# Kernel optimization log

Hardware: AMD Instinct MI355X
Metric: run time of the kernel (lower is better)

## Reference

```python
import jax, jax.numpy as jnp
import numpy as np

B, C, W, H = 4, 256, 128, 128
BLK = 16
D = C // 8


def setup_inputs() -> dict:
    key = jax.random.key(0)
    ks = jax.random.split(key, 7)
    s = 0.05
    return {
        "x": jax.random.normal(ks[0], (B, C, W, H), jnp.float32),
        "Wq": jax.random.normal(ks[1], (D, C), jnp.float32) * s,
        "bq": jax.random.normal(ks[2], (D,), jnp.float32) * s,
        "Wk": jax.random.normal(ks[3], (D, C), jnp.float32) * s,
        "bk": jax.random.normal(ks[4], (D,), jnp.float32) * s,
        "Wv": jax.random.normal(ks[5], (C, C), jnp.float32) * s,
        "bv": jax.random.normal(ks[6], (C,), jnp.float32) * s,
        "gamma": jnp.full((1,), 0.5, jnp.float32),
    }


def reference(x, Wq, bq, Wk, bk, Wv, bv, gamma):
    Bx, Cx, Wx, Hx = x.shape
    blk = BLK
    pw = (blk - Wx % blk) % blk
    ph = (blk - Hx % blk) % blk
    xp = jnp.pad(x, ((0, 0), (0, 0), (0, pw), (0, ph))) if (pw or ph) else x
    Wp, Hp = xp.shape[2], xp.shape[3]
    nW, nH = Wp // blk, Hp // blk
    N = blk * blk
    # partition into non-overlapping blk x blk windows -> (G, C, N)
    xb = xp.reshape(Bx, Cx, nW, blk, nH, blk).transpose(0, 2, 4, 1, 3, 5)
    xb = xb.reshape(-1, Cx, N)
    # padding mask: positions whose channel-abs-sum is zero are masked out
    mask = jnp.abs(xb).sum(axis=1) > 0  # (G, N) bool
    # 1x1 convs == per-pixel linear projections
    q = jnp.einsum('dc,gcn->gnd', Wq, xb) + bq            # (G, N, D)
    k = jnp.einsum('dc,gcn->gdn', Wk, xb) + bk[:, None]   # (G, D, N)
    energy = jnp.einsum('gnd,gdm->gnm', q, k)             # (G, N, N)
    NEG = jnp.float32(-1e9)
    energy = jnp.where(mask[:, None, :], energy, NEG)  # mask keys
    energy = jnp.where(mask[:, :, None], energy, NEG)  # mask queries
    att = jax.nn.softmax(energy, axis=-1)
    v = jnp.einsum('dc,gcn->gdn', Wv, xb) + bv[:, None]   # (G, C, N)
    out = jnp.einsum('gcm,gnm->gcn', v, att)              # (G, C, N)
    out = out.reshape(Bx, nW, nH, Cx, blk, blk).transpose(0, 3, 1, 4, 2, 5)
    out = out.reshape(Bx, Cx, Wp, Hp)[:, :, :Wx, :Hx]
    out = gamma * out + x
    return out, att
```

## Files before the change

kernel.cpp:

```cpp
#include <hip/hip_runtime.h>

typedef unsigned short u16;
typedef __attribute__((ext_vector_type(8))) short short8;
typedef __attribute__((ext_vector_type(4))) short s16x4;
typedef __attribute__((ext_vector_type(4))) float f32x4;

#define CC 256
#define WW 128
#define HH 128
#define DD 32
#define NN 256
#define WH (WW * HH)
#define P8 524288
#define OUTEL 16777216

__device__ __forceinline__ u16 f2bf(float f) {
  unsigned u = __float_as_uint(f);
  return (u16)((u + 0x7FFFu + ((u >> 16) & 1u)) >> 16);
}
__device__ __forceinline__ float bf2f(u16 h) {
  return __uint_as_float(((unsigned)h) << 16);
}

__global__ __launch_bounds__(256) void k_pack(const float* __restrict__ Wq,
                                              const float* __restrict__ Wk,
                                              float* __restrict__ wqk) {
  int idx = blockIdx.x * 256 + threadIdx.x;
  int r = idx >> 8, c = idx & 255;
  float v = (r < 32) ? Wq[r * 256 + c] : Wk[(r - 32) * 256 + c];
  wqk[c * 64 + r] = v;
}

__global__ __launch_bounds__(1024) void k_qk(const float* __restrict__ x,
                                             const float* __restrict__ wqk,
                                             const float* __restrict__ bq,
                                             const float* __restrict__ bk,
                                             u16* __restrict__ qk,
                                             u16* __restrict__ xbf) {
  __shared__ float xs[2][64 * 256];
  int hw = blockIdx.x;
  int g = (hw & 7) * 32 + (hw >> 3);
  int bb = g >> 6, wb = (g >> 3) & 7, hb = g & 7;
  int w0 = wb * 16, h0 = hb * 16;
  int t = threadIdx.x, ln = t & 63;
  int dg = __builtin_amdgcn_readfirstlane(t >> 6);
  int dq4 = dg & 7, is_k = dg >> 3;
  const float* xwin = x + (size_t)bb * CC * WH + (size_t)w0 * HH + h0;
  u16* xbg = xbf + (size_t)g * CC * NN;

  f32x4 st[4];
#pragma unroll
  for (int j = 0; j < 4; ++j) {
    int lin = j * 1024 + t;
    int c = lin >> 6, sub = lin & 63;
    st[j] = *(const f32x4*)(xwin + (size_t)c * WH + (sub >> 2) * HH + (sub & 3) * 4);
  }
#pragma unroll
  for (int j = 0; j < 4; ++j) {
    int lin = j * 1024 + t;
    int c = lin >> 6, sub = lin & 63;
    *(f32x4*)&xs[0][c * 256 + sub * 4] = st[j];
    s16x4 bp;
#pragma unroll
    for (int i = 0; i < 4; ++i) bp[i] = (short)f2bf(st[j][i]);
    *(s16x4*)&xbg[(size_t)c * NN + sub * 4] = bp;
  }

  float acc[4][4];
#pragma unroll
  for (int j = 0; j < 4; ++j)
#pragma unroll
    for (int i = 0; i < 4; ++i) acc[j][i] = 0.f;

  for (int s = 0; s < 4; ++s) {
    int nxt = s + 1;
    if (nxt < 4) {
#pragma unroll
      for (int j = 0; j < 4; ++j) {
        int lin = j * 1024 + t;
        int c = lin >> 6, sub = lin & 63;
        st[j] = *(const f32x4*)(xwin + (size_t)(nxt * 64 + c) * WH + (sub >> 2) * HH +
                                (sub & 3) * 4);
      }
    }
    __syncthreads();
    const float* xb = xs[s & 1];
    const float* wp = wqk + (s * 64) * 64 + dg * 4;
#pragma unroll 4
    for (int cc = 0; cc < 64; ++cc) {
      f32x4 xv = *(const f32x4*)(xb + cc * 256 + 4 * ln);
      f32x4 wv4 = *(const f32x4*)(wp + cc * 64);
#pragma unroll
      for (int j = 0; j < 4; ++j)
#pragma unroll
        for (int i = 0; i < 4; ++i) acc[j][i] = fmaf(wv4[j], xv[i], acc[j][i]);
    }
    if (nxt < 4) {
#pragma unroll
      for (int j = 0; j < 4; ++j) {
        int lin = j * 1024 + t;
        int c = lin >> 6, sub = lin & 63;
        *(f32x4*)&xs[nxt & 1][c * 256 + sub * 4] = st[j];
        s16x4 bp;
#pragma unroll
        for (int i = 0; i < 4; ++i) bp[i] = (short)f2bf(st[j][i]);
        *(s16x4*)&xbg[(size_t)(nxt * 64 + c) * NN + sub * 4] = bp;
      }
    }
  }

  const float* bsrc = is_k ? bk : bq;
  float bias[4];
#pragma unroll
  for (int j = 0; j < 4; ++j) bias[j] = bsrc[dq4 * 4 + j];

  u16* ph = qk + ((size_t)((is_k << 3) + (dq4 >> 1))) * P8;
  int sub = (dq4 & 1) * 4;
#pragma unroll
  for (int i = 0; i < 4; ++i) {
    int m = 4 * ln + i;
    s16x4 hv, lv;
#pragma unroll
    for (int j = 0; j < 4; ++j) {
      float v = acc[j][i] + bias[j];
      u16 h = f2bf(v);
      hv[j] = (short)h;
      lv[j] = (short)f2bf(v - bf2f(h));
    }
    size_t ro = (size_t)(g * NN + m) * 8 + sub;
    *(s16x4*)(ph + ro) = hv;
    *(s16x4*)(ph + 4 * (size_t)P8 + ro) = lv;
  }
}

__global__ __launch_bounds__(256, 4) void k_attn(const float* __restrict__ x,
                                                 const float* __restrict__ Wv,
                                                 const float* __restrict__ bv,
                                                 const u16* __restrict__ qk,
                                                 const u16* __restrict__ xbf,
                                                 const float* __restrict__ gamma,
                                                 float* __restrict__ dout) {
  __shared__ u16 tile[64 * 256];
  int hw = blockIdx.x;
  int L = (hw & 7) * 128 + (hw >> 3);
  int g = L >> 2, qt = L & 3;
  int bb = g >> 6, wb = (g >> 3) & 7, hb = g & 7;
  int w0 = wb * 16, h0 = hb * 16;
  int t = threadIdx.x, ln = t & 63, wv = t >> 6;
  float gam = gamma[0];
  float* attg = dout + (size_t)OUTEL;
  char* smem = (char*)tile;
  int n0 = qt * 64;
  int nt = n0 + wv * 16;
  int oct = ln >> 4;

  const u16* qb = qk + (size_t)oct * P8 + (size_t)(g * NN + nt + (ln & 15)) * 8;
  short8 ahi = *(const short8*)qb;
  short8 alo = *(const short8*)(qb + 4 * (size_t)P8);
  f32x4 e[16];
#pragma unroll
  for (int mt = 0; mt < 16; ++mt) e[mt] = (f32x4){0.f, 0.f, 0.f, 0.f};
#pragma unroll
  for (int mt = 0; mt < 16; ++mt) {
    const u16* kb = qk + (size_t)(8 + oct) * P8 + (size_t)(g * NN + mt * 16 + (ln & 15)) * 8;
    short8 bhi = *(const short8*)kb;
    short8 blo = *(const short8*)(kb + 4 * (size_t)P8);
    e[mt] = __builtin_amdgcn_mfma_f32_16x16x32_bf16(ahi, bhi, e[mt], 0, 0, 0);
    e[mt] = __builtin_amdgcn_mfma_f32_16x16x32_bf16(alo, bhi, e[mt], 0, 0, 0);
    e[mt] = __builtin_amdgcn_mfma_f32_16x16x32_bf16(ahi, blo, e[mt], 0, 0, 0);
  }

  float inv[4];
#pragma unroll
  for (int r = 0; r < 4; ++r) {
    float m0 = e[0][r];
#pragma unroll
    for (int mt = 1; mt < 16; ++mt) m0 = fmaxf(m0, e[mt][r]);
    m0 = fmaxf(m0, __shfl_xor(m0, 1));
    m0 = fmaxf(m0, __shfl_xor(m0, 2));
    m0 = fmaxf(m0, __shfl_xor(m0, 4));
    m0 = fmaxf(m0, __shfl_xor(m0, 8));
    float s = 0.f;
#pragma unroll
    for (int mt = 0; mt < 16; ++mt) {
      float p = __expf(e[mt][r] - m0);
      e[mt][r] = p;
      s += p;
    }
    s += __shfl_xor(s, 1);
    s += __shfl_xor(s, 2);
    s += __shfl_xor(s, 4);
    s += __shfl_xor(s, 8);
    inv[r] = 1.0f / s;
  }

#pragma unroll
  for (int mt = 0; mt < 16; ++mt)
#pragma unroll
    for (int r = 0; r < 4; ++r) {
      int nn = wv * 16 + (ln >> 4) * 4 + r;
      int m = mt * 16 + (ln & 15);
      int byteoff = nn * 512 + ((2 * m) ^ ((nn & 7) << 4));
      *(u16*)(smem + byteoff) = f2bf(e[mt][r] * inv[r]);
    }
  __syncthreads();

#pragma unroll
  for (int c = 0; c < 16; ++c) {
    int nn = c * 4 + (t >> 6);
    int m0 = 4 * (t & 63);
    int byteoff = nn * 512 + ((2 * m0) ^ ((nn & 7) << 4));
    s16x4 bv4 = *(const s16x4*)(smem + byteoff);
    f32x4 fv;
#pragma unroll
    for (int j = 0; j < 4; ++j) fv[j] = bf2f((u16)bv4[j]);
    *(f32x4*)(attg + (size_t)(g * NN + n0 + nn) * NN + m0) = fv;
  }

  int cbase = wv * 64;
  const u16* xbg = xbf + (size_t)g * CC * NN;
  f32x4 y[4][4];
#pragma unroll
  for (int ci = 0; ci < 4; ++ci)
#pragma unroll
    for (int ni = 0; ni < 4; ++ni) y[ci][ni] = (f32x4){0.f, 0.f, 0.f, 0.f};

#pragma unroll
  for (int kk = 0; kk < 8; ++kk) {
    short8 a[4];
#pragma unroll
    for (int ci = 0; ci < 4; ++ci)
      a[ci] = *(const short8*)&xbg[(size_t)(cbase + ci * 16 + (ln & 15)) * NN + kk * 32 +
                                   (ln >> 4) * 8];
    short8 bf[4];
#pragma unroll
    for (int ni = 0; ni < 4; ++ni) {
      int nn = ni * 16 + (ln & 15);
      int byteoff = nn * 512 + ((2 * (kk * 32 + (ln >> 4) * 8)) ^ ((nn & 7) << 4));
      bf[ni] = *(const short8*)(smem + byteoff);
    }
#pragma unroll
    for (int ci = 0; ci < 4; ++ci)
#pragma unroll
      for (int ni = 0; ni < 4; ++ni)
        y[ci][ni] = __builtin_amdgcn_mfma_f32_16x16x32_bf16(a[ci], bf[ni], y[ci][ni], 0, 0, 0);
  }
  __syncthreads();

#pragma unroll
  for (int ci = 0; ci < 4; ++ci)
#pragma unroll
    for (int ni = 0; ni < 4; ++ni)
#pragma unroll
      for (int r = 0; r < 4; ++r) {
        int nn = ni * 16 + (ln & 15);
        int cin = cbase + ci * 16 + (ln >> 4) * 4 + r;
        int byteoff = nn * 512 + ((2 * cin) ^ ((nn & 7) << 4));
        *(u16*)(smem + byteoff) = f2bf(y[ci][ni][r]);
      }
  __syncthreads();

  f32x4 o[4][4];
#pragma unroll
  for (int ci = 0; ci < 4; ++ci)
#pragma unroll
    for (int ni = 0; ni < 4; ++ni) o[ci][ni] = (f32x4){0.f, 0.f, 0.f, 0.f};

#pragma unroll
  for (int kk = 0; kk < 8; ++kk) {
    short8 wf[4];
#pragma unroll
    for (int ci = 0; ci < 4; ++ci) {
      int row = cbase + ci * 16 + (ln & 15);
      const float* wp = Wv + (size_t)row * CC + kk * 32 + (ln >> 4) * 8;
      f32x4 wa = *(const f32x4*)wp;
      f32x4 wb2 = *(const f32x4*)(wp + 4);
#pragma unroll
      for (int j = 0; j < 4; ++j) {
        wf[ci][j] = (short)f2bf(wa[j]);
        wf[ci][4 + j] = (short)f2bf(wb2[j]);
      }
    }
    short8 bf[4];
#pragma unroll
    for (int ni = 0; ni < 4; ++ni) {
      int nn = ni * 16 + (ln & 15);
      int byteoff = nn * 512 + ((2 * (kk * 32 + (ln >> 4) * 8)) ^ ((nn & 7) << 4));
      bf[ni] = *(const short8*)(smem + byteoff);
    }
#pragma unroll
    for (int ci = 0; ci < 4; ++ci)
#pragma unroll
      for (int ni = 0; ni < 4; ++ni)
        o[ci][ni] = __builtin_amdgcn_mfma_f32_16x16x32_bf16(wf[ci], bf[ni], o[ci][ni], 0, 0, 0);
  }

#pragma unroll
  for (int ci = 0; ci < 4; ++ci) {
    f32x4 bvv = *(const f32x4*)(bv + cbase + ci * 16 + (ln >> 4) * 4);
#pragma unroll
    for (int ni = 0; ni < 4; ++ni)
#pragma unroll
      for (int r = 0; r < 4; ++r) {
        int c = cbase + ci * 16 + (ln >> 4) * 4 + r;
        int n = n0 + ni * 16 + (ln & 15);
        size_t addr = (size_t)(bb * CC + c) * WH + (size_t)(w0 + (n >> 4)) * HH + h0 + (n & 15);
        dout[addr] = gam * (o[ci][ni][r] + bvv[r]) + x[addr];
      }
  }
}

extern "C" void kernel_launch(void* const* d_in, const int* in_sizes, int n_in,
                              void* d_out, int out_size, void* d_ws, size_t ws_size,
                              hipStream_t stream) {
  const float* x = (const float*)d_in[0];
  const float* Wq = (const float*)d_in[1];
  const float* bq = (const float*)d_in[2];
  const float* Wk = (const float*)d_in[3];
  const float* bk = (const float*)d_in[4];
  const float* Wv = (const float*)d_in[5];
  const float* bv = (const float*)d_in[6];
  const float* gamma = (const float*)d_in[7];
  float* out = (float*)d_out;

  float* wqk = (float*)d_ws;
  u16* qk = (u16*)((char*)d_ws + 65536);
  u16* xbf = qk + 16 * (size_t)P8;

  k_pack<<<64, 256, 0, stream>>>(Wq, Wk, wqk);
  k_qk<<<256, 1024, 0, stream>>>(x, wqk, bq, bk, qk, xbf);
  k_attn<<<1024, 256, 0, stream>>>(x, Wv, bv, qk, xbf, gamma, out);
}
```

Measured before the change: 292.4 us.

## Repartition x·att GEMM by query rows per wave to drop barriers

Each wave now computes the x·att^T product for its own 16 query rows across all 256 channels, reading only the attention rows it wrote itself. This removes two of the three __syncthreads and lets the attention write-out read back the wave's own rows. The intermediate y is written with vectorized 4-element stores instead of scalar u16 stores. In exchange each wave loads the full x tile from global memory (more global/L2 traffic per wave) and holds 16 accumulators.

```diff
diff --git a/kernel.cpp b/kernel.cpp
--- a/kernel.cpp
+++ b/kernel.cpp
@@ -151,7 +151,8 @@
   float* attg = dout + (size_t)OUTEL;
   char* smem = (char*)tile;
   int n0 = qt * 64;
-  int nt = n0 + wv * 16;
+  int nw = wv * 16;
+  int nt = n0 + nw;
   int oct = ln >> 4;
 
   const u16* qb = qk + (size_t)oct * P8 + (size_t)(g * NN + nt + (ln & 15)) * 8;
@@ -198,68 +199,61 @@
   for (int mt = 0; mt < 16; ++mt)
 #pragma unroll
     for (int r = 0; r < 4; ++r) {
-      int nn = wv * 16 + (ln >> 4) * 4 + r;
+      int nn = nw + (ln >> 4) * 4 + r;
       int m = mt * 16 + (ln & 15);
       int byteoff = nn * 512 + ((2 * m) ^ ((nn & 7) << 4));
       *(u16*)(smem + byteoff) = f2bf(e[mt][r] * inv[r]);
     }
-  __syncthreads();
-
-#pragma unroll
-  for (int c = 0; c < 16; ++c) {
-    int nn = c * 4 + (t >> 6);
-    int m0 = 4 * (t & 63);
-    int byteoff = nn * 512 + ((2 * m0) ^ ((nn & 7) << 4));
+
+  const u16* xbg = xbf + (size_t)g * CC * NN;
+  f32x4 y[16];
+#pragma unroll
+  for (int ci = 0; ci < 16; ++ci) y[ci] = (f32x4){0.f, 0.f, 0.f, 0.f};
+  {
+    int nnb = nw + (ln & 15);
+    int rowb = (ln & 15);
+    int qoff = (ln >> 4) * 8;
+#pragma unroll
+    for (int c4 = 0; c4 < 4; ++c4)
+#pragma unroll
+      for (int kk = 0; kk < 8; ++kk) {
+        int byteoff = nnb * 512 + ((2 * (kk * 32 + qoff)) ^ ((nnb & 7) << 4));
+        short8 bfr = *(const short8*)(smem + byteoff);
+#pragma unroll
+        for (int c2 = 0; c2 < 4; ++c2) {
+          int ci = c4 * 4 + c2;
+          short8 a = *(const short8*)&xbg[(size_t)(ci * 16 + rowb) * NN + kk * 32 + qoff];
+          y[ci] = __builtin_amdgcn_mfma_f32_16x16x32_bf16(a, bfr, y[ci], 0, 0, 0);
+        }
+      }
+  }
+
+#pragma unroll
+  for (int r16 = 0; r16 < 16; ++r16) {
+    int nn = nw + r16;
+    int byteoff = nn * 512 + ((8 * ln) ^ ((nn & 7) << 4));
     s16x4 bv4 = *(const s16x4*)(smem + byteoff);
     f32x4 fv;
 #pragma unroll
     for (int j = 0; j < 4; ++j) fv[j] = bf2f((u16)bv4[j]);
-    *(f32x4*)(attg + (size_t)(g * NN + n0 + nn) * NN + m0) = fv;
-  }
+    *(f32x4*)(attg + (size_t)(g * NN + n0 + nn) * NN + 4 * ln) = fv;
+  }
+
+  {
+    int nn2 = nw + (ln & 15);
+    int swz = (nn2 & 7) << 4;
+#pragma unroll
+    for (int ci = 0; ci < 16; ++ci) {
+      s16x4 h;
+#pragma unroll
+      for (int r = 0; r < 4; ++r) h[r] = (short)f2bf(y[ci][r]);
+      int byteoff = nn2 * 512 + ((32 * ci + 8 * (ln >> 4)) ^ swz);
+      *(s16x4*)(smem + byteoff) = h;
+    }
+  }
+  __syncthreads();
 
   int cbase = wv * 64;
-  const u16* xbg = xbf + (size_t)g * CC * NN;
-  f32x4 y[4][4];
-#pragma unroll
-  for (int ci = 0; ci < 4; ++ci)
-#pragma unroll
-    for (int ni = 0; ni < 4; ++ni) y[ci][ni] = (f32x4){0.f, 0.f, 0.f, 0.f};
-
-#pragma unroll
-  for (int kk = 0; kk < 8; ++kk) {
-    short8 a[4];
-#pragma unroll
-    for (int ci = 0; ci < 4; ++ci)
-      a[ci] = *(const short8*)&xbg[(size_t)(cbase + ci * 16 + (ln & 15)) * NN + kk * 32 +
-                                   (ln >> 4) * 8];
-    short8 bf[4];
-#pragma unroll
-    for (int ni = 0; ni < 4; ++ni) {
-      int nn = ni * 16 + (ln & 15);
-      int byteoff = nn * 512 + ((2 * (kk * 32 + (ln >> 4) * 8)) ^ ((nn & 7) << 4));
-      bf[ni] = *(const short8*)(smem + byteoff);
-    }
-#pragma unroll
-    for (int ci = 0; ci < 4; ++ci)
-#pragma unroll
-      for (int ni = 0; ni < 4; ++ni)
-        y[ci][ni] = __builtin_amdgcn_mfma_f32_16x16x32_bf16(a[ci], bf[ni], y[ci][ni], 0, 0, 0);
-  }
-  __syncthreads();
-
-#pragma unroll
-  for (int ci = 0; ci < 4; ++ci)
-#pragma unroll
-    for (int ni = 0; ni < 4; ++ni)
-#pragma unroll
-      for (int r = 0; r < 4; ++r) {
-        int nn = ni * 16 + (ln & 15);
-        int cin = cbase + ci * 16 + (ln >> 4) * 4 + r;
-        int byteoff = nn * 512 + ((2 * cin) ^ ((nn & 7) << 4));
-        *(u16*)(smem + byteoff) = f2bf(y[ci][ni][r]);
-      }
-  __syncthreads();
-
   f32x4 o[4][4];
 #pragma unroll
   for (int ci = 0; ci < 4; ++ci)
@@ -281,18 +275,18 @@
         wf[ci][4 + j] = (short)f2bf(wb2[j]);
       }
     }
-    short8 bf[4];
+    short8 bfr2[4];
 #pragma unroll
     for (int ni = 0; ni < 4; ++ni) {
       int nn = ni * 16 + (ln & 15);
       int byteoff = nn * 512 + ((2 * (kk * 32 + (ln >> 4) * 8)) ^ ((nn & 7) << 4));
-      bf[ni] = *(const short8*)(smem + byteoff);
+      bfr2[ni] = *(const short8*)(smem + byteoff);
     }
 #pragma unroll
     for (int ci = 0; ci < 4; ++ci)
 #pragma unroll
       for (int ni = 0; ni < 4; ++ni)
-        o[ci][ni] = __builtin_amdgcn_mfma_f32_16x16x32_bf16(wf[ci], bf[ni], o[ci][ni], 0, 0, 0);
+        o[ci][ni] = __builtin_amdgcn_mfma_f32_16x16x32_bf16(wf[ci], bfr2[ni], o[ci][ni], 0, 0, 0);
   }
 
 #pragma unroll
```

Result: slower. 332.1 us (+13.6%).
